# Kernel optimization log

Measured on AMD Instinct MI355X. Metric: run time of the kernel, lower is better.

## Reference

```python
import jax, jax.numpy as jnp
import numpy as np

K_MASK = -2.3819763e+38
ROTARY_DIM = 80        # int(128 * 0.625), already even
ROPE_THETA = 1000000.0
NORM_EPS = 1e-6


def apply_rope(x, positions, head_dim, rope_theta):
    # x: [B, T, n, head_dim]; positions: [B, T]
    fraction = 2.0 * jnp.arange(0, head_dim // 2, dtype=jnp.float32) / head_dim
    timescale = rope_theta ** fraction                      # [hd/2]
    sinusoid = positions.astype(jnp.float32)[..., None] / timescale[None, None, :]
    sinusoid = sinusoid[..., None, :]                       # [B, T, 1, hd/2]
    sin = jnp.sin(sinusoid).astype(x.dtype)
    cos = jnp.cos(sinusoid).astype(x.dtype)
    first, second = jnp.split(x, 2, axis=-1)
    return jnp.concatenate(
        [first * cos - second * sin, second * cos + first * sin], axis=-1
    ).astype(x.dtype)


def rms_norm(x, w, eps=NORM_EPS):
    # Qwen3.5 convention: x/rms * (1 + w), w zero-initialized
    out = x * jax.lax.rsqrt(jnp.mean(x * x, axis=-1, keepdims=True) + eps)
    return out * (1.0 + w)


def setup_inputs() -> dict:
    B, T, D, N, K, H = 4, 1024, 4096, 32, 8, 128
    key = jax.random.key(0)
    ks = jax.random.split(key, 5)
    return {
        "x": jax.random.normal(ks[0], (B, T, D), jnp.float32),
        "positions": jnp.tile(jnp.arange(T, dtype=jnp.int32)[None, :], (B, 1)),
        "wq": jax.random.normal(ks[1], (D, N, 2 * H), jnp.float32) * 0.02,
        "wk": jax.random.normal(ks[2], (D, K, H), jnp.float32) * 0.02,
        "wv": jax.random.normal(ks[3], (D, K, H), jnp.float32) * 0.02,
        "wo": jax.random.normal(ks[4], (N, H, D), jnp.float32) * 0.02,
        "q_norm_w": jnp.zeros((H,), jnp.float32),
        "k_norm_w": jnp.zeros((H,), jnp.float32),
    }


def reference(x, positions, wq, wk, wv, wo, q_norm_w, k_norm_w):
    H = wk.shape[-1]
    # QKV projections; q_proj produces head_dim*2 -> (query, sigmoid gate)
    qg = jnp.einsum('BTD,DNH->BTNH', x, wq)            # [B,T,N,2H]
    q, gate = jnp.split(qg, 2, axis=-1)                # [B,T,N,H] each
    k = jnp.einsum('BSD,DKH->BSKH', x, wk)             # [B,S,K,H]
    v = jnp.einsum('BSD,DKH->BSKH', x, wv)             # [B,S,K,H]
    # per-head RMSNorm (Qwen3.5 style)
    q = rms_norm(q, q_norm_w)
    k = rms_norm(k, k_norm_w)
    # partial RoPE on first ROTARY_DIM dims of each head
    q = jnp.concatenate(
        [apply_rope(q[..., :ROTARY_DIM], positions, ROTARY_DIM, ROPE_THETA),
         q[..., ROTARY_DIM:]], axis=-1)
    k = jnp.concatenate(
        [apply_rope(k[..., :ROTARY_DIM], positions, ROTARY_DIM, ROPE_THETA),
         k[..., ROTARY_DIM:]], axis=-1)
    B, T, N, _ = q.shape
    Kh = k.shape[2]
    G = N // Kh                                        # GQA group size
    qg5 = q.reshape(B, T, Kh, G, H)
    scores = jnp.einsum('BTKGH,BSKH->BKGTS', qg5, k) * (H ** -0.5)
    causal = jnp.tril(jnp.ones((T, T), dtype=bool))    # [T,S]
    scores = jnp.where(causal[None, None, None, :, :], scores, K_MASK)
    probs = jax.nn.softmax(scores, axis=-1)
    out = jnp.einsum('BKGTS,BSKH->BTKGH', probs, v).reshape(B, T, N, H)
    out = out * jax.nn.sigmoid(gate)                   # gated attention output
    return jnp.einsum('BTNH,NHD->BTD', out, wo)
```

## Files before the change

### kernel.cpp

```cpp
#include <hip/hip_runtime.h>
#include <cstdint>
#include <cstddef>


typedef __attribute__((ext_vector_type(8))) short short8;
typedef __attribute__((ext_vector_type(4))) float float4v;

__device__ __forceinline__ unsigned short f2bf(float f) {
  unsigned u = __builtin_bit_cast(unsigned, f);
  u += 0x7fffu + ((u >> 16) & 1u);
  return (unsigned short)(u >> 16);
}
__device__ __forceinline__ float bf2f(unsigned short h) {
  unsigned u = ((unsigned)h) << 16;
  return __builtin_bit_cast(float, u);
}

__device__ __forceinline__ void gload_lds16(const void* g, void* l) {
  typedef const __attribute__((address_space(1))) void as1_cv;
  typedef __attribute__((address_space(3))) void as3_v;
  __builtin_amdgcn_global_load_lds((as1_cv*)g, (as3_v*)l, 16, 0, 0);
}

__global__ __launch_bounds__(256) void transpose_cvt(
    const float* __restrict__ src, unsigned short* __restrict__ dst,
    int R, int C) {
  __shared__ float tile[32][33];
  const int c0 = blockIdx.x * 32, r0 = blockIdx.y * 32;
  for (int i = threadIdx.y; i < 32; i += 8)
    tile[i][threadIdx.x] = src[(size_t)(r0 + i) * C + c0 + threadIdx.x];
  __syncthreads();
  for (int i = threadIdx.y; i < 32; i += 8)
    dst[(size_t)(c0 + i) * R + r0 + threadIdx.x] = f2bf(tile[threadIdx.x][i]);
}

__global__ __launch_bounds__(256) void cvt_f32_bf16(
    const float* __restrict__ src, unsigned short* __restrict__ dst, int n4) {
  int i = blockIdx.x * blockDim.x + threadIdx.x;
  if (i >= n4) return;
  float4 f = ((const float4*)src)[i];
  ushort4 o;
  o.x = f2bf(f.x); o.y = f2bf(f.y); o.z = f2bf(f.z); o.w = f2bf(f.w);
  ((ushort4*)dst)[i] = o;
}

__global__ __launch_bounds__(256) void v_transpose(
    const unsigned short* __restrict__ qkv, unsigned short* __restrict__ vtb) {
  __shared__ unsigned short tile[64][65];
  const int t0 = blockIdx.x * 64, h0 = blockIdx.y * 64;
  const int bk = blockIdx.z, b = bk >> 3, kh = bk & 7;
  const int tx = threadIdx.x & 63, ty = threadIdx.x >> 6;
  const unsigned short* src =
      qkv + (size_t)(b * 1024 + t0) * 10240 + 9216 + kh * 128 + h0;
  for (int i = ty; i < 64; i += 4)
    tile[i][tx] = src[(size_t)i * 10240 + tx];
  __syncthreads();
  unsigned short* dst = vtb + ((size_t)bk * 128 + h0) * 1024 + t0;
  for (int i = ty; i < 64; i += 4)
    dst[(size_t)i * 1024 + tx] = tile[tx][i];
}

template <bool BF16OUT>
__global__ __launch_bounds__(256) void gemm_bt(
    const unsigned short* __restrict__ A, const unsigned short* __restrict__ BT,
    void* __restrict__ Cv, int M, int N, int Kd) {
  constexpr int BK = 64;
  __shared__ unsigned short As[128 * BK];
  __shared__ unsigned short Bs[128 * BK];

  const int tid = threadIdx.x;
  const int lane = tid & 63;
  const int wv = tid >> 6;
  const int wr = wv >> 1, wc = wv & 1;
  const int m0 = blockIdx.y * 128, n0 = blockIdx.x * 128;
  const int ml = lane & 15, q = lane >> 4;

  const int r0 = tid >> 3;
  const int cSw = ((tid & 7) ^ (r0 & 7)) * 8;
  const unsigned short* gA = A + (size_t)(m0 + r0) * Kd + cSw;
  const unsigned short* gB = BT + (size_t)(n0 + r0) * Kd + cSw;
  unsigned short* lA = &As[r0 * BK + (tid & 7) * 8];
  unsigned short* lB = &Bs[r0 * BK + (tid & 7) * 8];

  float4v acc[4][4];
#pragma unroll
  for (int i = 0; i < 4; ++i)
#pragma unroll
    for (int j = 0; j < 4; ++j) acc[i][j] = (float4v)0.0f;

  for (int k0 = 0; k0 < Kd; k0 += BK) {
#pragma unroll
    for (int it = 0; it < 4; ++it) {
      gload_lds16(gA + (size_t)it * 32 * Kd + k0, lA + it * 32 * BK);
      gload_lds16(gB + (size_t)it * 32 * Kd + k0, lB + it * 32 * BK);
    }
    __syncthreads();
#pragma unroll
    for (int ks = 0; ks < 2; ++ks) {
      short8 af[4], bfr[4];
      const int csw = ((ks * 4 + q) ^ (ml & 7)) * 8;
#pragma unroll
      for (int i = 0; i < 4; ++i)
        af[i] = *(const short8*)&As[(wr * 64 + i * 16 + ml) * BK + csw];
#pragma unroll
      for (int j = 0; j < 4; ++j)
        bfr[j] = *(const short8*)&Bs[(wc * 64 + j * 16 + ml) * BK + csw];
#pragma unroll
      for (int i = 0; i < 4; ++i)
#pragma unroll
        for (int j = 0; j < 4; ++j)
          acc[i][j] = __builtin_amdgcn_mfma_f32_16x16x32_bf16(af[i], bfr[j], acc[i][j], 0, 0, 0);
    }
    __syncthreads();
  }

#pragma unroll
  for (int i = 0; i < 4; ++i) {
#pragma unroll
    for (int j = 0; j < 4; ++j) {
      const int grow = m0 + wr * 64 + i * 16 + q * 4;
      const int gcol = n0 + wc * 64 + j * 16 + ml;
#pragma unroll
      for (int r = 0; r < 4; ++r) {
        size_t idx = (size_t)(grow + r) * N + gcol;
        if constexpr (BF16OUT)
          ((unsigned short*)Cv)[idx] = f2bf(acc[i][j][r]);
        else
          ((float*)Cv)[idx] = acc[i][j][r];
      }
    }
  }
}

__global__ __launch_bounds__(256) void postproc_kernel(
    const unsigned short* __restrict__ qkv, const int* __restrict__ positions,
    const float* __restrict__ qnw, const float* __restrict__ knw,
    unsigned short* __restrict__ q_rot, unsigned short* __restrict__ sgb,
    unsigned short* __restrict__ k_rot) {
  const int wave = threadIdx.x >> 6, lane = threadIdx.x & 63;
  const int gslot = blockIdx.x * 4 + wave;
  const int m = gslot / 40, hs = gslot % 40;
  const int b = m >> 10, t = m & 1023;

  const unsigned short* base = (hs < 32)
      ? qkv + (size_t)m * 10240 + hs * 256
      : qkv + (size_t)m * 10240 + 8192 + (hs - 32) * 128;

  float v1 = bf2f(base[lane]);
  float v2 = bf2f(base[64 + lane]);

  float ss = v1 * v1 + v2 * v2;
  for (int off = 32; off > 0; off >>= 1) ss += __shfl_xor(ss, off);
  const float r = rsqrtf(ss * (1.0f / 128.0f) + 1e-6f);
  const float* nw = (hs < 32) ? qnw : knw;
  v1 *= r * (1.0f + nw[lane]);
  v2 *= r * (1.0f + nw[64 + lane]);

  const float pos = (float)positions[m];
  const int i1 = (lane < 40) ? lane : lane - 40;
  const float ang1 = pos * expf(-0.3453877639491068f * (float)i1);
  const float s1 = sinf(ang1), c1 = cosf(ang1);
  const float ang2 = pos * expf(-0.3453877639491068f * (float)(lane + 24));
  const float s2 = sinf(ang2), c2 = cosf(ang2);

  const float shA1 = __shfl(v1, (lane + 40) & 63);
  const float shA2 = __shfl(v2, (lane + 40) & 63);
  const float shX = __shfl(v1, (lane + 24) & 63);
  const float pA = (lane < 24) ? shA1 : shA2;
  const float o1 = (lane < 40) ? (v1 * c1 - pA * s1) : (v1 * c1 + shX * s1);
  const float o2 = (lane < 16) ? (v2 * c2 + shX * s2) : v2;

  if (hs < 32) {
    size_t qb = ((size_t)m * 32 + hs) * 128;
    q_rot[qb + lane] = f2bf(o1);
    q_rot[qb + 64 + lane] = f2bf(o2);
    float g1 = bf2f(base[128 + lane]), g2 = bf2f(base[192 + lane]);
    sgb[qb + lane] = f2bf(1.0f / (1.0f + expf(-g1)));
    sgb[qb + 64 + lane] = f2bf(1.0f / (1.0f + expf(-g2)));
  } else {
    const int kh = hs - 32;
    size_t kb = ((size_t)(b * 8 + kh) * 1024 + t) * 128;
    k_rot[kb + lane] = f2bf(o1);
    k_rot[kb + 64 + lane] = f2bf(o2);
  }
}

__global__ __launch_bounds__(256) void attn_kernel(
    const unsigned short* __restrict__ q_rot, const unsigned short* __restrict__ k_rot,
    const unsigned short* __restrict__ vt, const unsigned short* __restrict__ sgate,
    unsigned short* __restrict__ attn_out) {
  __shared__ unsigned short Ks[64 * 128];
  __shared__ unsigned short Vts[128 * 64];
  __shared__ unsigned short Ps[64 * 72];

  const int tid = threadIdx.x;
  const int lane = tid & 63, w = tid >> 6;
  const int qt = blockIdx.x & 15;
  const int n = (blockIdx.x >> 4) & 31;
  const int b = blockIdx.x >> 9;
  const int kh = n >> 2;
  const int t0 = qt * 64;
  const int ml = lane & 15, q = lane >> 4;
  const float SCALE = 0.08838834764831845f;

  short8 aq[4];
  {
    const unsigned short* qp =
        q_rot + (((size_t)(b * 1024 + t0 + w * 16 + ml)) * 32 + n) * 128 + q * 8;
#pragma unroll
    for (int ks = 0; ks < 4; ++ks) aq[ks] = *(const short8*)(qp + ks * 32);
  }

  float4v O[8];
#pragma unroll
  for (int i = 0; i < 8; ++i) O[i] = (float4v)0.0f;
  float mrow[4] = {-3e38f, -3e38f, -3e38f, -3e38f};
  float lrow[4] = {0.f, 0.f, 0.f, 0.f};

  const unsigned short* kbase = k_rot + (size_t)(b * 8 + kh) * 1024 * 128;
  const unsigned short* vbase = vt + (size_t)(b * 8 + kh) * 128 * 1024;
  const int rK = tid >> 4, cK = tid & 15;
  const int cKsw = (cK ^ rK) * 8;
  const int rV = tid >> 3, cV = tid & 7;
  const int cVsw = (cV ^ (rV & 7)) * 8;

  for (int si = 0; si <= qt; ++si) {
    const int s0 = si * 64;
#pragma unroll
    for (int it = 0; it < 4; ++it) {
      const int li = it * 256 + tid;
      gload_lds16(kbase + (size_t)(s0 + rK + it * 16) * 128 + cKsw, &Ks[li * 8]);
      gload_lds16(vbase + (size_t)(rV + it * 32) * 1024 + s0 + cVsw, &Vts[li * 8]);
    }
    __syncthreads();

    float4v Sv[4];
#pragma unroll
    for (int j = 0; j < 4; ++j) Sv[j] = (float4v)0.0f;
#pragma unroll
    for (int ks = 0; ks < 4; ++ks) {
#pragma unroll
      for (int j = 0; j < 4; ++j) {
        short8 bk = *(const short8*)&Ks[(j * 16 + ml) * 128 + (((ks * 4 + q) ^ ml) * 8)];
        Sv[j] = __builtin_amdgcn_mfma_f32_16x16x32_bf16(aq[ks], bk, Sv[j], 0, 0, 0);
      }
    }

    float P[4][4];
#pragma unroll
    for (int rr = 0; rr < 4; ++rr) {
      const int tg = t0 + w * 16 + q * 4 + rr;
      float vmax = -3e38f;
#pragma unroll
      for (int j = 0; j < 4; ++j) {
        const int sj = s0 + j * 16 + ml;
        float v = Sv[j][rr] * SCALE;
        if (sj > tg) v = -3.0e38f;
        P[j][rr] = v;
        vmax = fmaxf(vmax, v);
      }
      for (int off = 1; off < 16; off <<= 1) vmax = fmaxf(vmax, __shfl_xor(vmax, off));
      const float mnew = fmaxf(mrow[rr], vmax);
      const float alpha = __expf(mrow[rr] - mnew);
      mrow[rr] = mnew;
      lrow[rr] *= alpha;
#pragma unroll
      for (int ht = 0; ht < 8; ++ht) O[ht][rr] *= alpha;
      float rsum = 0.f;
#pragma unroll
      for (int j = 0; j < 4; ++j) {
        float e = __expf(P[j][rr] - mnew);
        P[j][rr] = e;
        rsum += e;
      }
      for (int off = 1; off < 16; off <<= 1) rsum += __shfl_xor(rsum, off);
      lrow[rr] += rsum;
    }

#pragma unroll
    for (int rr = 0; rr < 4; ++rr)
#pragma unroll
      for (int j = 0; j < 4; ++j)
        Ps[(w * 16 + q * 4 + rr) * 72 + j * 16 + ml] = f2bf(P[j][rr]);

#pragma unroll
    for (int ks = 0; ks < 2; ++ks) {
      short8 ap = *(const short8*)&Ps[(w * 16 + ml) * 72 + ks * 32 + q * 8];
#pragma unroll
      for (int ht = 0; ht < 8; ++ht) {
        short8 bv = *(const short8*)&Vts[(ht * 16 + ml) * 64 + (((ks * 4 + q) ^ (ml & 7)) * 8)];
        O[ht] = __builtin_amdgcn_mfma_f32_16x16x32_bf16(ap, bv, O[ht], 0, 0, 0);
      }
    }
    __syncthreads();
  }

#pragma unroll
  for (int rr = 0; rr < 4; ++rr) {
    const int tg = t0 + w * 16 + q * 4 + rr;
    const size_t ob = ((size_t)(b * 1024 + tg) * 32 + n) * 128;
    const float inv = 1.0f / lrow[rr];
#pragma unroll
    for (int ht = 0; ht < 8; ++ht) {
      const int h = ht * 16 + ml;
      attn_out[ob + h] = f2bf(O[ht][rr] * inv * bf2f(sgate[ob + h]));
    }
  }
}

extern "C" void kernel_launch(void* const* d_in, const int* in_sizes, int n_in,
                              void* d_out, int out_size, void* d_ws, size_t ws_size,
                              hipStream_t stream) {
  (void)in_sizes; (void)n_in; (void)out_size; (void)ws_size;
  const float* x = (const float*)d_in[0];
  const int* pos = (const int*)d_in[1];
  const float* wq = (const float*)d_in[2];
  const float* wk = (const float*)d_in[3];
  const float* wv = (const float*)d_in[4];
  const float* wo = (const float*)d_in[5];
  const float* qnw = (const float*)d_in[6];
  const float* knw = (const float*)d_in[7];
  float* out = (float*)d_out;

  unsigned short* ws = (unsigned short*)d_ws;
  unsigned short* x_bf = ws;
  unsigned short* wT = x_bf + 16777216;
  unsigned short* woT = wT + 41943040;
  unsigned short* qkv = woT + 16777216;
  unsigned short* q_rot = qkv + 41943040;
  unsigned short* sgb = q_rot + 16777216;
  unsigned short* k_rot = sgb + 16777216;
  unsigned short* vtb = k_rot + 4194304;
  unsigned short* attn = wT;

  dim3 tb(32, 8);
  transpose_cvt<<<dim3(256, 128), tb, 0, stream>>>(wq, wT, 4096, 8192);
  transpose_cvt<<<dim3(32, 128), tb, 0, stream>>>(wk, wT + (size_t)8192 * 4096, 4096, 1024);
  transpose_cvt<<<dim3(32, 128), tb, 0, stream>>>(wv, wT + (size_t)9216 * 4096, 4096, 1024);
  transpose_cvt<<<dim3(128, 128), tb, 0, stream>>>(wo, woT, 4096, 4096);
  cvt_f32_bf16<<<16384, 256, 0, stream>>>(x, x_bf, 4194304);

  gemm_bt<true><<<dim3(80, 32), 256, 0, stream>>>(x_bf, wT, (void*)qkv, 4096, 10240, 4096);
  postproc_kernel<<<40960, 256, 0, stream>>>(qkv, pos, qnw, knw, q_rot, sgb, k_rot);
  v_transpose<<<dim3(16, 2, 32), 256, 0, stream>>>(qkv, vtb);
  attn_kernel<<<2048, 256, 0, stream>>>(q_rot, k_rot, vtb, sgb, attn);
  gemm_bt<false><<<dim3(32, 32), 256, 0, stream>>>(attn, woT, (void*)out, 4096, 4096, 4096);
}
```

Measured before the change: 1.136 ms.

## Replace GEMM with 256x256-tile, 4-stage pipelined LDS kernel using 8 waves

Rewrites both projection GEMMs to use 256x256 output tiles with 512 threads, a K-step of 32 and a 4-deep LDS ring buffer. Global-to-LDS loads are issued three tiles ahead and interleaved with MFMA phases, using explicit vmcnt waits, barriers and setprio. The goal is to hide memory latency and raise data reuse per tile. In exchange, LDS use grows to 128KB and register pressure rises, and the larger tiles leave the output GEMM with only 256 blocks, so fewer workgroups are in flight.

```diff
diff --git a/kernel.cpp b/kernel.cpp
--- a/kernel.cpp
+++ b/kernel.cpp
@@ -61,64 +61,111 @@
 }
 
 template <bool BF16OUT>
-__global__ __launch_bounds__(256) void gemm_bt(
+__global__ __launch_bounds__(512, 2) void gemm_bt256(
     const unsigned short* __restrict__ A, const unsigned short* __restrict__ BT,
     void* __restrict__ Cv, int M, int N, int Kd) {
-  constexpr int BK = 64;
-  __shared__ unsigned short As[128 * BK];
-  __shared__ unsigned short Bs[128 * BK];
+  __shared__ unsigned short As[4][256 * 32];
+  __shared__ unsigned short Bs[4][256 * 32];
 
   const int tid = threadIdx.x;
   const int lane = tid & 63;
   const int wv = tid >> 6;
-  const int wr = wv >> 1, wc = wv & 1;
-  const int m0 = blockIdx.y * 128, n0 = blockIdx.x * 128;
+  const int wr = wv >> 2, wc = wv & 3;
+  const int m0 = blockIdx.y * 256, n0 = blockIdx.x * 256;
   const int ml = lane & 15, q = lane >> 4;
 
-  const int r0 = tid >> 3;
-  const int cSw = ((tid & 7) ^ (r0 & 7)) * 8;
-  const unsigned short* gA = A + (size_t)(m0 + r0) * Kd + cSw;
-  const unsigned short* gB = BT + (size_t)(n0 + r0) * Kd + cSw;
-  unsigned short* lA = &As[r0 * BK + (tid & 7) * 8];
-  unsigned short* lB = &Bs[r0 * BK + (tid & 7) * 8];
-
-  float4v acc[4][4];
-#pragma unroll
-  for (int i = 0; i < 4; ++i)
+  const int sr = tid >> 2;
+  const int pc = tid & 3;
+  const int gc = (pc ^ (sr & 3)) * 8;
+  const unsigned short* gA0 = A + (size_t)(m0 + sr) * Kd + gc;
+  const unsigned short* gB0 = BT + (size_t)(n0 + sr) * Kd + gc;
+  const unsigned short* gA1 = gA0 + (size_t)128 * Kd;
+  const unsigned short* gB1 = gB0 + (size_t)128 * Kd;
+  const int lo0 = tid * 8;
+  const int lo1 = 4096 + tid * 8;
+
+  const int rdc = (q ^ (ml & 3)) * 8;
+  const int aOff = (wr * 128 + ml) * 32 + rdc;
+  const int bOff = (wc * 64 + ml) * 32 + rdc;
+
+  float4v acc[8][4];
+#pragma unroll
+  for (int i = 0; i < 8; ++i)
 #pragma unroll
     for (int j = 0; j < 4; ++j) acc[i][j] = (float4v)0.0f;
 
-  for (int k0 = 0; k0 < Kd; k0 += BK) {
-#pragma unroll
-    for (int it = 0; it < 4; ++it) {
-      gload_lds16(gA + (size_t)it * 32 * Kd + k0, lA + it * 32 * BK);
-      gload_lds16(gB + (size_t)it * 32 * Kd + k0, lB + it * 32 * BK);
-    }
-    __syncthreads();
-#pragma unroll
-    for (int ks = 0; ks < 2; ++ks) {
-      short8 af[4], bfr[4];
-      const int csw = ((ks * 4 + q) ^ (ml & 7)) * 8;
-#pragma unroll
-      for (int i = 0; i < 4; ++i)
-        af[i] = *(const short8*)&As[(wr * 64 + i * 16 + ml) * BK + csw];
+  const int NT = Kd >> 5;
+
+#pragma unroll
+  for (int t = 0; t < 3; ++t) {
+    gload_lds16(gA0 + t * 32, &As[t][lo0]);
+    gload_lds16(gA1 + t * 32, &As[t][lo1]);
+    gload_lds16(gB0 + t * 32, &Bs[t][lo0]);
+    gload_lds16(gB1 + t * 32, &Bs[t][lo1]);
+  }
+  asm volatile("s_waitcnt vmcnt(8)" ::: "memory");
+  __builtin_amdgcn_s_barrier();
+
+  for (int T = 0; T < NT; ++T) {
+    const int buf = T & 3;
+    const bool doStage = (T + 3 < NT);
+    const int sb = (T + 3) & 3;
+    const int gk = (T + 3) * 32;
+
+    short8 bfr[4], af[4];
+#pragma unroll
+    for (int j = 0; j < 4; ++j)
+      bfr[j] = *(const short8*)&Bs[buf][bOff + j * 512];
+#pragma unroll
+    for (int i = 0; i < 4; ++i)
+      af[i] = *(const short8*)&As[buf][aOff + i * 512];
+    if (doStage) {
+      gload_lds16(gA0 + gk, &As[sb][lo0]);
+      gload_lds16(gB0 + gk, &Bs[sb][lo0]);
+    }
+    __builtin_amdgcn_s_barrier();
+    asm volatile("s_waitcnt lgkmcnt(0)" ::: "memory");
+    __builtin_amdgcn_sched_barrier(0);
+    __builtin_amdgcn_s_setprio(1);
+#pragma unroll
+    for (int i = 0; i < 4; ++i)
 #pragma unroll
       for (int j = 0; j < 4; ++j)
-        bfr[j] = *(const short8*)&Bs[(wc * 64 + j * 16 + ml) * BK + csw];
-#pragma unroll
-      for (int i = 0; i < 4; ++i)
-#pragma unroll
-        for (int j = 0; j < 4; ++j)
-          acc[i][j] = __builtin_amdgcn_mfma_f32_16x16x32_bf16(af[i], bfr[j], acc[i][j], 0, 0, 0);
-    }
-    __syncthreads();
-  }
-
-#pragma unroll
-  for (int i = 0; i < 4; ++i) {
+        acc[i][j] = __builtin_amdgcn_mfma_f32_16x16x32_bf16(af[i], bfr[j], acc[i][j], 0, 0, 0);
+    __builtin_amdgcn_s_setprio(0);
+    __builtin_amdgcn_s_barrier();
+
+#pragma unroll
+    for (int i = 0; i < 4; ++i)
+      af[i] = *(const short8*)&As[buf][aOff + 2048 + i * 512];
+    if (doStage) {
+      gload_lds16(gA1 + gk, &As[sb][lo1]);
+      gload_lds16(gB1 + gk, &Bs[sb][lo1]);
+    }
+    __builtin_amdgcn_s_barrier();
+    asm volatile("s_waitcnt lgkmcnt(0)" ::: "memory");
+    __builtin_amdgcn_sched_barrier(0);
+    __builtin_amdgcn_s_setprio(1);
+#pragma unroll
+    for (int i = 0; i < 4; ++i)
+#pragma unroll
+      for (int j = 0; j < 4; ++j)
+        acc[4 + i][j] = __builtin_amdgcn_mfma_f32_16x16x32_bf16(af[i], bfr[j], acc[4 + i][j], 0, 0, 0);
+    __builtin_amdgcn_s_setprio(0);
+    if (T + 3 < NT)
+      asm volatile("s_waitcnt vmcnt(8)" ::: "memory");
+    else if (T + 2 < NT)
+      asm volatile("s_waitcnt vmcnt(4)" ::: "memory");
+    else if (T + 1 < NT)
+      asm volatile("s_waitcnt vmcnt(0)" ::: "memory");
+    __builtin_amdgcn_s_barrier();
+  }
+
+#pragma unroll
+  for (int i = 0; i < 8; ++i) {
 #pragma unroll
     for (int j = 0; j < 4; ++j) {
-      const int grow = m0 + wr * 64 + i * 16 + q * 4;
+      const int grow = m0 + wr * 128 + i * 16 + q * 4;
       const int gcol = n0 + wc * 64 + j * 16 + ml;
 #pragma unroll
       for (int r = 0; r < 4; ++r) {
@@ -340,9 +387,9 @@
   transpose_cvt<<<dim3(128, 128), tb, 0, stream>>>(wo, woT, 4096, 4096);
   cvt_f32_bf16<<<16384, 256, 0, stream>>>(x, x_bf, 4194304);
 
-  gemm_bt<true><<<dim3(80, 32), 256, 0, stream>>>(x_bf, wT, (void*)qkv, 4096, 10240, 4096);
+  gemm_bt256<true><<<dim3(40, 16), 512, 0, stream>>>(x_bf, wT, (void*)qkv, 4096, 10240, 4096);
   postproc_kernel<<<40960, 256, 0, stream>>>(qkv, pos, qnw, knw, q_rot, sgb, k_rot);
   v_transpose<<<dim3(16, 2, 32), 256, 0, stream>>>(qkv, vtb);
   attn_kernel<<<2048, 256, 0, stream>>>(q_rot, k_rot, vtb, sgb, attn);
-  gemm_bt<false><<<dim3(32, 32), 256, 0, stream>>>(attn, woT, (void*)out, 4096, 4096, 4096);
-}
+  gemm_bt256<false><<<dim3(16, 16), 512, 0, stream>>>(attn, woT, (void*)out, 4096, 4096, 4096);
+}
```

New measurement: 1.129 ms. About the same (-0.7%).

## Replace GEMM with 256x256-tile, 8-wave, double-buffered pipelined MFMA kernel

Applied to the files above, without the earlier changes.

Replaces the 128x128 single-buffered bf16 GEMM used for the QKV and output projections with a 256x256 tile kernel. It runs 512 threads, double-buffers LDS and interleaves global-to-LDS loads, LDS reads and MFMA phases using explicit waitcnt, barriers and setprio. The goal is to hide memory latency behind matrix math and raise data reuse per tile. In exchange it uses more LDS and registers, and the grid has fewer blocks (256 for the output GEMM), which may underfill the 256 CUs.

```diff
diff --git a/kernel.cpp b/kernel.cpp
--- a/kernel.cpp
+++ b/kernel.cpp
@@ -61,64 +61,164 @@
 }
 
 template <bool BF16OUT>
-__global__ __launch_bounds__(256) void gemm_bt(
+__global__ __launch_bounds__(512, 2) void gemm_bt256(
     const unsigned short* __restrict__ A, const unsigned short* __restrict__ BT,
     void* __restrict__ Cv, int M, int N, int Kd) {
-  constexpr int BK = 64;
-  __shared__ unsigned short As[128 * BK];
-  __shared__ unsigned short Bs[128 * BK];
+  __shared__ unsigned short As[2][16384];
+  __shared__ unsigned short Bs[2][16384];
 
   const int tid = threadIdx.x;
   const int lane = tid & 63;
   const int wv = tid >> 6;
-  const int wr = wv >> 1, wc = wv & 1;
-  const int m0 = blockIdx.y * 128, n0 = blockIdx.x * 128;
+  const int wr = wv >> 2, wc = wv & 3;
+  const int m0 = blockIdx.y * 256, n0 = blockIdx.x * 256;
   const int ml = lane & 15, q = lane >> 4;
 
-  const int r0 = tid >> 3;
-  const int cSw = ((tid & 7) ^ (r0 & 7)) * 8;
-  const unsigned short* gA = A + (size_t)(m0 + r0) * Kd + cSw;
-  const unsigned short* gB = BT + (size_t)(n0 + r0) * Kd + cSw;
-  unsigned short* lA = &As[r0 * BK + (tid & 7) * 8];
-  unsigned short* lB = &Bs[r0 * BK + (tid & 7) * 8];
-
-  float4v acc[4][4];
-#pragma unroll
-  for (int i = 0; i < 4; ++i)
+  const int srow = tid >> 3;
+  const int sgc = ((tid & 7) ^ (srow & 7)) * 8;
+  const unsigned short* gAs = A + (size_t)(m0 + srow) * Kd + sgc;
+  const unsigned short* gBs = BT + (size_t)(n0 + srow) * Kd + sgc;
+  const size_t r64K = (size_t)64 * Kd, r128K = (size_t)128 * Kd;
+  const int ls = tid * 8;
+
+  const int rch = (q ^ (ml & 7)) * 8;
+  const int aBase = (wr * 128 + ml) * 64 + rch;
+  const int bBase = (wc * 64 + ml) * 64 + rch;
+
+  float4v acc[8][4];
+#pragma unroll
+  for (int i = 0; i < 8; ++i)
 #pragma unroll
     for (int j = 0; j < 4; ++j) acc[i][j] = (float4v)0.0f;
 
-  for (int k0 = 0; k0 < Kd; k0 += BK) {
-#pragma unroll
-    for (int it = 0; it < 4; ++it) {
-      gload_lds16(gA + (size_t)it * 32 * Kd + k0, lA + it * 32 * BK);
-      gload_lds16(gB + (size_t)it * 32 * Kd + k0, lB + it * 32 * BK);
-    }
-    __syncthreads();
-#pragma unroll
-    for (int ks = 0; ks < 2; ++ks) {
-      short8 af[4], bfr[4];
-      const int csw = ((ks * 4 + q) ^ (ml & 7)) * 8;
-#pragma unroll
-      for (int i = 0; i < 4; ++i)
-        af[i] = *(const short8*)&As[(wr * 64 + i * 16 + ml) * BK + csw];
-#pragma unroll
-      for (int j = 0; j < 4; ++j)
-        bfr[j] = *(const short8*)&Bs[(wc * 64 + j * 16 + ml) * BK + csw];
-#pragma unroll
-      for (int i = 0; i < 4; ++i)
-#pragma unroll
-        for (int j = 0; j < 4; ++j)
-          acc[i][j] = __builtin_amdgcn_mfma_f32_16x16x32_bf16(af[i], bfr[j], acc[i][j], 0, 0, 0);
-    }
-    __syncthreads();
-  }
-
-#pragma unroll
-  for (int i = 0; i < 4; ++i) {
+  const int NI = Kd >> 7;
+
+  short8 af0[8], af1[8], b0[4], b1[4];
+
+#define STG_A(bf, h, col) do {                                            \
+    gload_lds16(gAs + (size_t)(h) * r128K + (col), &As[bf][(h)*8192 + ls]); \
+    gload_lds16(gAs + (size_t)(h) * r128K + r64K + (col),                  \
+                &As[bf][(h)*8192 + 4096 + ls]);                            \
+  } while (0)
+#define STG_B(bf, h, col) do {                                            \
+    gload_lds16(gBs + (size_t)(h) * r128K + (col), &Bs[bf][(h)*8192 + ls]); \
+    gload_lds16(gBs + (size_t)(h) * r128K + r64K + (col),                  \
+                &Bs[bf][(h)*8192 + 4096 + ls]);                            \
+  } while (0)
+#define READ_AF(DST, BUFP, QM) do {                                       \
+    _Pragma("unroll")                                                     \
+    for (int ii = 0; ii < 4; ++ii) {                                      \
+      DST[ii*2]   = *(const short8*)&(BUFP)[aBase + (QM)*4096 + ii*1024]; \
+      DST[ii*2+1] = *(const short8*)&(BUFP)[(aBase + (QM)*4096 + ii*1024) ^ 32]; \
+    } } while (0)
+#define READ_BF(DST, BUFP, QN) do {                                       \
+    _Pragma("unroll")                                                     \
+    for (int jj = 0; jj < 2; ++jj) {                                      \
+      DST[jj*2]   = *(const short8*)&(BUFP)[bBase + (QN)*2048 + jj*1024]; \
+      DST[jj*2+1] = *(const short8*)&(BUFP)[(bBase + (QN)*2048 + jj*1024) ^ 32]; \
+    } } while (0)
+#define MFMA_Q(AF, BF, R0, C0) do {                                       \
+    _Pragma("unroll")                                                     \
+    for (int ks = 0; ks < 2; ++ks)                                        \
+      _Pragma("unroll")                                                   \
+      for (int ii = 0; ii < 4; ++ii)                                      \
+        _Pragma("unroll")                                                 \
+        for (int jj = 0; jj < 2; ++jj)                                    \
+          acc[(R0)+ii][(C0)+jj] = __builtin_amdgcn_mfma_f32_16x16x32_bf16( \
+              AF[ii*2+ks], BF[jj*2+ks], acc[(R0)+ii][(C0)+jj], 0, 0, 0);  \
+  } while (0)
+#define PH_MID(NLG) do {                                                  \
+    __builtin_amdgcn_sched_barrier(0);                                    \
+    __builtin_amdgcn_s_barrier();                                         \
+    asm volatile("s_waitcnt lgkmcnt(" #NLG ")" ::: "memory");             \
+    __builtin_amdgcn_sched_barrier(0);                                    \
+    __builtin_amdgcn_s_setprio(1);                                        \
+  } while (0)
+#define PH_END() do {                                                     \
+    __builtin_amdgcn_s_setprio(0);                                        \
+    __builtin_amdgcn_s_barrier();                                         \
+  } while (0)
+
+  STG_A(0, 0, 0); STG_A(0, 1, 0); STG_B(0, 0, 0); STG_B(0, 1, 0);
+  STG_A(1, 0, 64);
+  asm volatile("s_waitcnt vmcnt(2)" ::: "memory");
+  __builtin_amdgcn_s_barrier();
+  READ_AF(af0, As[0], 0);
+
+  for (int i = 0; i < NI; ++i) {
+    const int c1 = i * 128 + 64, c2 = i * 128 + 128, c3 = i * 128 + 192;
+    const bool more = (i + 1 < NI);
+
+    READ_BF(b0, Bs[0], 0); READ_BF(b1, Bs[0], 1);
+    STG_A(1, 1, c1);
+    PH_MID(4);
+    MFMA_Q(af0, b0, 0, 0);
+    PH_END();
+
+    READ_AF(af1, As[0], 1);
+    STG_B(1, 0, c1);
+    PH_MID(8);
+    MFMA_Q(af0, b1, 0, 2);
+    PH_END();
+
+    STG_B(1, 1, c1);
+    asm volatile("s_waitcnt vmcnt(4)" ::: "memory");
+    PH_MID(0);
+    MFMA_Q(af1, b0, 4, 0);
+    PH_END();
+
+    READ_AF(af0, As[1], 0);
+    if (more) {
+      STG_A(0, 0, c2);
+      asm volatile("s_waitcnt vmcnt(2)" ::: "memory");
+    } else {
+      asm volatile("s_waitcnt vmcnt(0)" ::: "memory");
+    }
+    PH_MID(8);
+    MFMA_Q(af1, b1, 4, 2);
+    PH_END();
+
+    READ_BF(b0, Bs[1], 0); READ_BF(b1, Bs[1], 1);
+    if (more) STG_A(0, 1, c2);
+    PH_MID(4);
+    MFMA_Q(af0, b0, 0, 0);
+    PH_END();
+
+    READ_AF(af1, As[1], 1);
+    if (more) STG_B(0, 0, c2);
+    PH_MID(8);
+    MFMA_Q(af0, b1, 0, 2);
+    PH_END();
+
+    if (more) STG_B(0, 1, c2);
+    asm volatile("s_waitcnt vmcnt(4)" ::: "memory");
+    PH_MID(0);
+    MFMA_Q(af1, b0, 4, 0);
+    PH_END();
+
+    if (more) {
+      READ_AF(af0, As[0], 0);
+      STG_A(1, 0, c3);
+    }
+    asm volatile("s_waitcnt vmcnt(2)" ::: "memory");
+    PH_MID(8);
+    MFMA_Q(af1, b1, 4, 2);
+    PH_END();
+  }
+
+#undef STG_A
+#undef STG_B
+#undef READ_AF
+#undef READ_BF
+#undef MFMA_Q
+#undef PH_MID
+#undef PH_END
+
+#pragma unroll
+  for (int i = 0; i < 8; ++i) {
 #pragma unroll
     for (int j = 0; j < 4; ++j) {
-      const int grow = m0 + wr * 64 + i * 16 + q * 4;
+      const int grow = m0 + wr * 128 + i * 16 + q * 4;
       const int gcol = n0 + wc * 64 + j * 16 + ml;
 #pragma unroll
       for (int r = 0; r < 4; ++r) {
@@ -340,9 +440,9 @@
   transpose_cvt<<<dim3(128, 128), tb, 0, stream>>>(wo, woT, 4096, 4096);
   cvt_f32_bf16<<<16384, 256, 0, stream>>>(x, x_bf, 4194304);
 
-  gemm_bt<true><<<dim3(80, 32), 256, 0, stream>>>(x_bf, wT, (void*)qkv, 4096, 10240, 4096);
+  gemm_bt256<true><<<dim3(40, 16), 512, 0, stream>>>(x_bf, wT, (void*)qkv, 4096, 10240, 4096);
   postproc_kernel<<<40960, 256, 0, stream>>>(qkv, pos, qnw, knw, q_rot, sgb, k_rot);
   v_transpose<<<dim3(16, 2, 32), 256, 0, stream>>>(qkv, vtb);
   attn_kernel<<<2048, 256, 0, stream>>>(q_rot, k_rot, vtb, sgb, attn);
-  gemm_bt<false><<<dim3(32, 32), 256, 0, stream>>>(attn, woT, (void*)out, 4096, 4096, 4096);
-}
+  gemm_bt256<false><<<dim3(16, 16), 512, 0, stream>>>(attn, woT, (void*)out, 4096, 4096, 4096);
+}
```

Measured after the change: 1.455 ms. 1.28x slower.
